# Kernel optimization log

Hardware: AMD Instinct MI355X
Metric: run time of the kernel (lower is better)

The kernel has to match this reference:

```python
import jax, jax.numpy as jnp
import numpy as np

NUM_HEADS = 8  # from init_kwargs

def _conv1x1(x, W, b):
    # x: [B, Cin, H, W], W: [Cout, Cin], b: [Cout]  (nn.Conv2d kernel_size=1)
    return jnp.einsum('bchw,oc->bohw', x, W) + b[None, :, None, None]

def setup_inputs() -> dict:
    key = jax.random.key(0)
    ks = jax.random.split(key, 9)
    B, C, H, W = 8, 256, 32, 32
    Ck, Cv, Co = 256, 256, 256
    s = 1.0 / np.sqrt(C)
    return {
        'x':  jax.random.normal(ks[0], (B, C, H, W), dtype=jnp.float32),
        'Wq': jax.random.normal(ks[1], (Ck, C), dtype=jnp.float32) * s,
        'bq': jax.random.normal(ks[2], (Ck,), dtype=jnp.float32) * 0.02,
        'Wk': jax.random.normal(ks[3], (Ck, C), dtype=jnp.float32) * s,
        'bk': jax.random.normal(ks[4], (Ck,), dtype=jnp.float32) * 0.02,
        'Wv': jax.random.normal(ks[5], (Cv, C), dtype=jnp.float32) * s,
        'bv': jax.random.normal(ks[6], (Cv,), dtype=jnp.float32) * 0.02,
        'Wo': jax.random.normal(ks[7], (Co, Cv), dtype=jnp.float32) * s,
        'bo': jax.random.normal(ks[8], (Co,), dtype=jnp.float32) * 0.02,
    }

def reference(x, Wq, bq, Wk, bk, Wv, bv, Wo, bo):
    B, C, H, W = x.shape
    q = _conv1x1(x, Wq, bq)  # [B, Ck, H, W]
    k = _conv1x1(x, Wk, bk)  # [B, Ck, H, W]
    v = _conv1x1(x, Wv, bv)  # [B, Cv, H, W]
    nh = NUM_HEADS
    dk = q.shape[1] // nh
    dv = v.shape[1] // nh
    N = H * W
    # split heads, flatten spatial dims into sequence
    q = q.reshape(B, nh, dk, N) * (dk ** -0.5)
    k = k.reshape(B, nh, dk, N)
    v = v.reshape(B, nh, dv, N)
    logits = jnp.einsum('bhdn,bhdm->bhnm', q, k)        # [B, nh, N, N]
    attn = jax.nn.softmax(logits, axis=-1)
    o = jnp.einsum('bhnm,bhdm->bhdn', attn, v)           # [B, nh, dv, N]
    o = o.reshape(B, nh * dv, H, W)
    return _conv1x1(o, Wo, bo)                           # [B, Co, H, W]
```

## Files before the change

### kernel.cpp

```cpp
#include <hip/hip_runtime.h>
#include <math.h>

typedef unsigned short u16;
typedef __attribute__((ext_vector_type(8))) unsigned short u16x8;
typedef __attribute__((ext_vector_type(8))) short s16x8;
typedef __attribute__((ext_vector_type(4))) float f32x4;

#define QK_SCALE (0.17677669529663687f * 1.4426950408889634f)

__device__ __forceinline__ unsigned cvt2(float lo, float hi) {
  unsigned r;
  asm("v_cvt_pk_bf16_f32 %0, %1, %2" : "=v"(r) : "v"(lo), "v"(hi));
  return r;
}
__device__ __forceinline__ u16 f2bf(float f) { return (u16)cvt2(f, f); }
__device__ __forceinline__ u16x8 ld16(const void* p) { u16x8 v; __builtin_memcpy(&v, p, 16); return v; }
__device__ __forceinline__ void st16(void* p, u16x8 v) { __builtin_memcpy(p, &v, 16); }
__device__ __forceinline__ void st4(void* p, unsigned v) { __builtin_memcpy(p, &v, 4); }
__device__ __forceinline__ void st8(void* p, unsigned lo, unsigned hi) {
  unsigned long long v = ((unsigned long long)hi << 32) | (unsigned long long)lo;
  __builtin_memcpy(p, &v, 8);
}
__device__ __forceinline__ f32x4 ldf4(const void* p) { f32x4 v; __builtin_memcpy(&v, p, 16); return v; }
__device__ __forceinline__ s16x8 frag16(const void* p) { s16x8 v; __builtin_memcpy(&v, p, 16); return v; }
__device__ __forceinline__ s16x8 pack8(f32x4 lo, f32x4 hi) {
  union { unsigned u[4]; s16x8 s; } c;
  c.u[0] = cvt2(lo.x, lo.y); c.u[1] = cvt2(lo.z, lo.w);
  c.u[2] = cvt2(hi.x, hi.y); c.u[3] = cvt2(hi.z, hi.w);
  return c.s;
}

__global__ __launch_bounds__(256) void r27_qkv(
    const float* __restrict__ x,
    const float* __restrict__ Wq, const float* __restrict__ bq,
    const float* __restrict__ Wk, const float* __restrict__ bk,
    const float* __restrict__ Wv, const float* __restrict__ bv,
    u16* __restrict__ qo, u16* __restrict__ ko, u16* __restrict__ vo)
{
  __shared__ u16 xt[64][264];
  __shared__ u16 wlds[192][40];

  const int t = threadIdx.x;
  const int ntile = blockIdx.x, hp = blockIdx.y, b = blockIdx.z;
  const int n0 = ntile * 64, h0 = hp * 2;
  const int w = t >> 6, lane = t & 63, l15 = lane & 15, quad = lane >> 4;
  const int oct = t & 7;

  {
    const int i = t & 15, co = t >> 4;
    const float* xb = x + ((size_t)b * 256 + co) * 1024 + n0 + i * 4;
    const int msk = (i & 7) << 3;
#pragma unroll
    for (int p = 0; p < 16; ++p) {
      const f32x4 a = ldf4(xb + (size_t)p * 16 * 1024);
      const int c = p * 16 + co;
#pragma unroll
      for (int j = 0; j < 4; ++j)
        xt[i * 4 + j][(c ^ msk)] = f2bf(a[j]);
    }
  }

  f32x4 acc[12];
#pragma unroll
  for (int i = 0; i < 12; ++i) acc[i] = (f32x4){0.f, 0.f, 0.f, 0.f};

  for (int ks = 0; ks < 8; ++ks) {
    __syncthreads();
    {
#pragma unroll
      for (int u = 0; u < 6; ++u) {
        const int row = (u * 256 + t) >> 3;
        const int m = row >> 6, hh = (row >> 5) & 1, rr = row & 31;
        const float* M = (m == 0) ? Wq : (m == 1) ? Wk : Wv;
        const f32x4 a = ldf4(M + (size_t)((h0 + hh) * 32 + rr) * 256
                             + ks * 32 + oct * 4);
        st8(&wlds[row][oct * 4], cvt2(a.x, a.y), cvt2(a.z, a.w));
      }
    }
    __syncthreads();

    const int nrow = w * 16 + l15;
    const s16x8 bfrag = frag16(
        &xt[nrow][(ks * 32 + quad * 8) ^ (((nrow >> 2) & 7) << 3)]);
#pragma unroll
    for (int mt = 0; mt < 12; ++mt) {
      const s16x8 af = frag16(&wlds[mt * 16 + l15][quad * 8]);
      acc[mt] = __builtin_amdgcn_mfma_f32_16x16x32_bf16(af, bfrag, acc[mt], 0, 0, 0);
    }
  }

  const int n = n0 + w * 16 + l15;
  const int sig = n & 127;
  const int ntn = sig >> 4, q4 = (sig >> 2) & 3, rn = sig & 3;
  const int nperm = (n & ~127) | ((ntn >> 1) << 5) | (q4 << 3) | ((ntn & 1) << 2) | rn;
#pragma unroll
  for (int hh = 0; hh < 2; ++hh) {
    const int h = h0 + hh;
    const size_t bh = (size_t)(b * 8 + h);
    u16* qrow = qo + (bh * 1024 + n) * 32;
    u16* krow = ko + (bh * 1024 + n) * 32;
#pragma unroll
    for (int half = 0; half < 2; ++half) {
      const int d0 = half * 16 + quad * 4;
      const f32x4 aq = acc[0 + hh * 2 + half];
      const f32x4 ak = acc[4 + hh * 2 + half];
      const f32x4 av = acc[8 + hh * 2 + half];
      st4(qrow + d0,     cvt2((aq.x + bq[h * 32 + d0 + 0]) * QK_SCALE,
                              (aq.y + bq[h * 32 + d0 + 1]) * QK_SCALE));
      st4(qrow + d0 + 2, cvt2((aq.z + bq[h * 32 + d0 + 2]) * QK_SCALE,
                              (aq.w + bq[h * 32 + d0 + 3]) * QK_SCALE));
      st4(krow + d0,     cvt2(ak.x + bk[h * 32 + d0 + 0],
                              ak.y + bk[h * 32 + d0 + 1]));
      st4(krow + d0 + 2, cvt2(ak.z + bk[h * 32 + d0 + 2],
                              ak.w + bk[h * 32 + d0 + 3]));
#pragma unroll
      for (int rr = 0; rr < 4; ++rr) {
        const int d = d0 + rr;
        vo[(bh * 32 + d) * 1024 + nperm] = f2bf(av[rr] + bv[h * 32 + d]);
      }
    }
  }
}

__global__ __launch_bounds__(256) void r27_attn(
    const u16* __restrict__ qw, const u16* __restrict__ kw,
    const u16* __restrict__ vw, u16* __restrict__ ows)
{
  __shared__ u16 klds[128][40];
  __shared__ u16 vlds[32][136];

  const int t = threadIdx.x;
  const int qtile = blockIdx.x;
  const int bh = blockIdx.y;
  const int w = t >> 6, lane = t & 63, l15 = lane & 15, quad = lane >> 4;

  const s16x8 qfrag = frag16(
      qw + ((size_t)bh * 1024 + qtile * 64 + w * 16 + l15) * 32 + quad * 8);

  const u16* kbase = kw + ((size_t)bh * 1024 + (t >> 1)) * 32 + (t & 1) * 16;
  const u16* vbase = vw + ((size_t)bh * 32 + (t >> 3)) * 1024 + (t & 7) * 16;

  u16x8 gk0 = ld16(kbase), gk1 = ld16(kbase + 8);
  u16x8 gv0 = ld16(vbase), gv1 = ld16(vbase + 8);

  f32x4 o0 = {0.f, 0.f, 0.f, 0.f}, o1 = {0.f, 0.f, 0.f, 0.f};
  float mrun = -1e30f, lrun = 0.f;

  for (int kb = 0; kb < 8; ++kb) {
    if (kb) __syncthreads();
    st16(&klds[t >> 1][(t & 1) * 16], gk0);
    st16(&klds[t >> 1][(t & 1) * 16 + 8], gk1);
    st16(&vlds[t >> 3][(t & 7) * 16], gv0);
    st16(&vlds[t >> 3][(t & 7) * 16 + 8], gv1);
    if (kb < 7) {
      const u16* kn = kbase + (size_t)(kb + 1) * (128 * 32);
      const u16* vn = vbase + (size_t)(kb + 1) * 128;
      gk0 = ld16(kn); gk1 = ld16(kn + 8);
      gv0 = ld16(vn); gv1 = ld16(vn + 8);
    }
    __syncthreads();

    f32x4 s[8];
    const f32x4 zz = {0.f, 0.f, 0.f, 0.f};
#pragma unroll
    for (int nt2 = 0; nt2 < 8; ++nt2) {
      const s16x8 kf = frag16(&klds[nt2 * 16 + l15][quad * 8]);
      s[nt2] = __builtin_amdgcn_mfma_f32_16x16x32_bf16(kf, qfrag, zz, 0, 0, 0);
    }

    float mx = fmaxf(fmaxf(s[0][0], s[0][1]), fmaxf(s[0][2], s[0][3]));
#pragma unroll
    for (int nt2 = 1; nt2 < 8; ++nt2)
      mx = fmaxf(mx, fmaxf(fmaxf(s[nt2][0], s[nt2][1]),
                           fmaxf(s[nt2][2], s[nt2][3])));
    mx = fmaxf(mx, __shfl_xor(mx, 16));
    mx = fmaxf(mx, __shfl_xor(mx, 32));
    const float mnew = fmaxf(mrun, mx);
    const float alpha = exp2f(mrun - mnew);
    float rs = 0.f;
#pragma unroll
    for (int nt2 = 0; nt2 < 8; ++nt2) {
#pragma unroll
      for (int r = 0; r < 4; ++r) {
        s[nt2][r] = exp2f(s[nt2][r] - mnew);
        rs += s[nt2][r];
      }
    }
    rs += __shfl_xor(rs, 16);
    rs += __shfl_xor(rs, 32);
    lrun = lrun * alpha + rs;
    mrun = mnew;
#pragma unroll
    for (int r = 0; r < 4; ++r) { o0[r] *= alpha; o1[r] *= alpha; }

#pragma unroll
    for (int ks = 0; ks < 4; ++ks) {
      const s16x8 pf  = pack8(s[2 * ks], s[2 * ks + 1]);
      const s16x8 vf0 = frag16(&vlds[l15][ks * 32 + quad * 8]);
      const s16x8 vf1 = frag16(&vlds[16 + l15][ks * 32 + quad * 8]);
      o0 = __builtin_amdgcn_mfma_f32_16x16x32_bf16(vf0, pf, o0, 0, 0, 0);
      o1 = __builtin_amdgcn_mfma_f32_16x16x32_bf16(vf1, pf, o1, 0, 0, 0);
    }
  }

  const float inv = 1.0f / lrun;
  const int b = bh >> 3, hh = bh & 7;
  u16* obase = ows + ((size_t)b * 1024 + qtile * 64 + w * 16 + l15) * 256
             + hh * 32 + quad * 4;
  st8(obase,      cvt2(o0[0] * inv, o0[1] * inv), cvt2(o0[2] * inv, o0[3] * inv));
  st8(obase + 16, cvt2(o1[0] * inv, o1[1] * inv), cvt2(o1[2] * inv, o1[3] * inv));
}

__global__ __launch_bounds__(256) void r27_oproj(
    const u16* __restrict__ ows,
    const float* __restrict__ Wo, const float* __restrict__ bo,
    float* __restrict__ out)
{
  __shared__ u16 o2t[32][256];
  __shared__ u16 wl3[2][256][40];

  const int t = threadIdx.x;
  const int nt = blockIdx.x, b = blockIdx.y;
  const int w = t >> 6, lane = t & 63, l15 = lane & 15, quad = lane >> 4;
  const int oct = t & 7;

  {
    const int g = t & 31, nr = t >> 5;
#pragma unroll
    for (int p = 0; p < 4; ++p) {
      const int n = p * 8 + nr;
      const u16* src = ows + ((size_t)b * 1024 + nt * 32 + n) * 256 + g * 8;
      st16(&o2t[n][(g ^ (n & 7)) << 3], ld16(src));
    }
  }

  auto stage_wo = [&](int ks, int buf) {
#pragma unroll
    for (int u = 0; u < 8; ++u) {
      const int row = u * 32 + (t >> 3);
      const f32x4 a = ldf4(Wo + (size_t)row * 256 + ks * 32 + oct * 4);
      st8(&wl3[buf][row][oct * 4], cvt2(a.x, a.y), cvt2(a.z, a.w));
    }
  };

  stage_wo(0, 0);
  __syncthreads();

  f32x4 acc[4][2];
#pragma unroll
  for (int mt = 0; mt < 4; ++mt) {
    acc[mt][0] = (f32x4){0.f, 0.f, 0.f, 0.f};
    acc[mt][1] = (f32x4){0.f, 0.f, 0.f, 0.f};
  }

  const int m0 = l15 & 7;

  for (int ks = 0; ks < 8; ++ks) {
    if (ks < 7) stage_wo(ks + 1, (ks + 1) & 1);
    const s16x8 b0 = frag16(&o2t[l15][((ks * 4 + quad) ^ m0) << 3]);
    const s16x8 b1 = frag16(&o2t[16 + l15][((ks * 4 + quad) ^ m0) << 3]);
#pragma unroll
    for (int mt = 0; mt < 4; ++mt) {
      const s16x8 af = frag16(&wl3[ks & 1][w * 64 + mt * 16 + l15][quad * 8]);
      acc[mt][0] = __builtin_amdgcn_mfma_f32_16x16x32_bf16(af, b0, acc[mt][0], 0, 0, 0);
      acc[mt][1] = __builtin_amdgcn_mfma_f32_16x16x32_bf16(af, b1, acc[mt][1], 0, 0, 0);
    }
    __syncthreads();
  }

#pragma unroll
  for (int mt = 0; mt < 4; ++mt) {
#pragma unroll
    for (int r = 0; r < 4; ++r) {
      const int oc = w * 64 + mt * 16 + quad * 4 + r;
      const float bov = bo[oc];
      out[((size_t)b * 256 + oc) * 1024 + nt * 32 + l15]      = acc[mt][0][r] + bov;
      out[((size_t)b * 256 + oc) * 1024 + nt * 32 + 16 + l15] = acc[mt][1][r] + bov;
    }
  }
}

extern "C" void kernel_launch(void* const* d_in, const int* in_sizes, int n_in,
                              void* d_out, int out_size, void* d_ws, size_t ws_size,
                              hipStream_t stream) {
  (void)in_sizes; (void)n_in; (void)out_size; (void)ws_size;
  const float* x  = (const float*)d_in[0];
  const float* Wq = (const float*)d_in[1];
  const float* bq = (const float*)d_in[2];
  const float* Wk = (const float*)d_in[3];
  const float* bk = (const float*)d_in[4];
  const float* Wv = (const float*)d_in[5];
  const float* bv = (const float*)d_in[6];
  const float* Wo = (const float*)d_in[7];
  const float* bo = (const float*)d_in[8];
  float* out = (float*)d_out;

  char* ws = (char*)d_ws;
  u16* qw  = (u16*)(ws);
  u16* kw  = (u16*)(ws + (4u << 20));
  u16* vw  = (u16*)(ws + (8u << 20));
  u16* ows = (u16*)(ws + (12u << 20));

  r27_qkv<<<dim3(16, 4, 8), 256, 0, stream>>>(
      x, Wq, bq, Wk, bk, Wv, bv, qw, kw, vw);
  r27_attn<<<dim3(16, 64), 256, 0, stream>>>(qw, kw, vw, ows);
  r27_oproj<<<dim3(32, 8), 256, 0, stream>>>(ows, Wo, bo, out);
}
```

Measured before the change: 128.1 us.

## Fuse output projection into attention kernel via last-arriver counter

Removes the separate output-projection launch. Each attention block bumps an atomic counter per (batch, query tile), and the eighth head block to arrive performs the Wo projection for that 64-column tile, reusing the shared memory. Wo staging moves from a double-buffered LDS scheme to register prefetch with a single LDS buffer. In exchange it adds a memset launch, threadfences and atomics, and leaves the projection work serialized on only 128 winning blocks at the tail of the attention kernel.

```diff
diff --git a/kernel.cpp b/kernel.cpp
--- a/kernel.cpp
+++ b/kernel.cpp
@@ -30,7 +30,7 @@
   return c.s;
 }
 
-__global__ __launch_bounds__(256) void r27_qkv(
+__global__ __launch_bounds__(256) void r28_qkv(
     const float* __restrict__ x,
     const float* __restrict__ Wq, const float* __restrict__ bq,
     const float* __restrict__ Wk, const float* __restrict__ bk,
@@ -122,12 +122,17 @@
   }
 }
 
-__global__ __launch_bounds__(256) void r27_attn(
+__global__ __launch_bounds__(256) void r28_attn_oproj(
     const u16* __restrict__ qw, const u16* __restrict__ kw,
-    const u16* __restrict__ vw, u16* __restrict__ ows)
+    const u16* __restrict__ vw,
+    const float* __restrict__ Wo, const float* __restrict__ bo,
+    u16* __restrict__ ows, float* __restrict__ out,
+    unsigned* __restrict__ cnt)
 {
-  __shared__ u16 klds[128][40];
-  __shared__ u16 vlds[32][136];
+  __shared__ __align__(16) char smem[36864];
+  __shared__ int winflag;
+  u16 (*klds)[40]  = (u16(*)[40])smem;
+  u16 (*vlds)[136] = (u16(*)[136])(smem + 10240);
 
   const int t = threadIdx.x;
   const int qtile = blockIdx.x;
@@ -209,73 +214,89 @@
              + hh * 32 + quad * 4;
   st8(obase,      cvt2(o0[0] * inv, o0[1] * inv), cvt2(o0[2] * inv, o0[3] * inv));
   st8(obase + 16, cvt2(o1[0] * inv, o1[1] * inv), cvt2(o1[2] * inv, o1[3] * inv));
-}
-
-__global__ __launch_bounds__(256) void r27_oproj(
-    const u16* __restrict__ ows,
-    const float* __restrict__ Wo, const float* __restrict__ bo,
-    float* __restrict__ out)
-{
-  __shared__ u16 o2t[32][256];
-  __shared__ u16 wl3[2][256][40];
-
-  const int t = threadIdx.x;
-  const int nt = blockIdx.x, b = blockIdx.y;
-  const int w = t >> 6, lane = t & 63, l15 = lane & 15, quad = lane >> 4;
-  const int oct = t & 7;
-
-  {
-    const int g = t & 31, nr = t >> 5;
-#pragma unroll
-    for (int p = 0; p < 4; ++p) {
-      const int n = p * 8 + nr;
-      const u16* src = ows + ((size_t)b * 1024 + nt * 32 + n) * 256 + g * 8;
-      st16(&o2t[n][(g ^ (n & 7)) << 3], ld16(src));
-    }
-  }
-
-  auto stage_wo = [&](int ks, int buf) {
+
+  __syncthreads();
+  __threadfence();
+  if (t == 0)
+    winflag = (atomicAdd(&cnt[b * 16 + qtile], 1u) == 7u) ? 1 : 0;
+  __syncthreads();
+  if (!winflag) return;
+  __threadfence();
+
+  u16 (*o2t)[256] = (u16(*)[256])smem;
+  u16 (*wl)[40]   = (u16(*)[40])(smem + 16384);
+
+  const int rr = t >> 3, oct = t & 7;
+  const float* wsrc = Wo + (size_t)rr * 256 + oct * 4;
+  const int m0 = l15 & 7;
+
+  for (int half = 0; half < 2; ++half) {
+    const int nt = qtile * 2 + half;
+    __syncthreads();
+    {
+      const int g = t & 31, nr = t >> 5;
+#pragma unroll
+      for (int p = 0; p < 4; ++p) {
+        const int n = p * 8 + nr;
+        const u16* src = ows + ((size_t)b * 1024 + nt * 32 + n) * 256 + g * 8;
+        st16(&o2t[n][(g ^ (n & 7)) << 3], ld16(src));
+      }
+    }
+    unsigned wreg[8][2];
 #pragma unroll
     for (int u = 0; u < 8; ++u) {
-      const int row = u * 32 + (t >> 3);
-      const f32x4 a = ldf4(Wo + (size_t)row * 256 + ks * 32 + oct * 4);
-      st8(&wl3[buf][row][oct * 4], cvt2(a.x, a.y), cvt2(a.z, a.w));
-    }
-  };
-
-  stage_wo(0, 0);
-  __syncthreads();
-
-  f32x4 acc[4][2];
-#pragma unroll
-  for (int mt = 0; mt < 4; ++mt) {
-    acc[mt][0] = (f32x4){0.f, 0.f, 0.f, 0.f};
-    acc[mt][1] = (f32x4){0.f, 0.f, 0.f, 0.f};
-  }
-
-  const int m0 = l15 & 7;
-
-  for (int ks = 0; ks < 8; ++ks) {
-    if (ks < 7) stage_wo(ks + 1, (ks + 1) & 1);
-    const s16x8 b0 = frag16(&o2t[l15][((ks * 4 + quad) ^ m0) << 3]);
-    const s16x8 b1 = frag16(&o2t[16 + l15][((ks * 4 + quad) ^ m0) << 3]);
+      const f32x4 a = ldf4(wsrc + (size_t)u * 32 * 256);
+      wreg[u][0] = cvt2(a.x, a.y); wreg[u][1] = cvt2(a.z, a.w);
+    }
+
+    f32x4 acc[4][2];
 #pragma unroll
     for (int mt = 0; mt < 4; ++mt) {
-      const s16x8 af = frag16(&wl3[ks & 1][w * 64 + mt * 16 + l15][quad * 8]);
-      acc[mt][0] = __builtin_amdgcn_mfma_f32_16x16x32_bf16(af, b0, acc[mt][0], 0, 0, 0);
-      acc[mt][1] = __builtin_amdgcn_mfma_f32_16x16x32_bf16(af, b1, acc[mt][1], 0, 0, 0);
-    }
-    __syncthreads();
-  }
-
-#pragma unroll
-  for (int mt = 0; mt < 4; ++mt) {
-#pragma unroll
-    for (int r = 0; r < 4; ++r) {
-      const int oc = w * 64 + mt * 16 + quad * 4 + r;
-      const float bov = bo[oc];
-      out[((size_t)b * 256 + oc) * 1024 + nt * 32 + l15]      = acc[mt][0][r] + bov;
-      out[((size_t)b * 256 + oc) * 1024 + nt * 32 + 16 + l15] = acc[mt][1][r] + bov;
+      acc[mt][0] = (f32x4){0.f, 0.f, 0.f, 0.f};
+      acc[mt][1] = (f32x4){0.f, 0.f, 0.f, 0.f};
+    }
+
+    for (int ks = 0; ks < 8; ++ks) {
+      __syncthreads();
+#pragma unroll
+      for (int u = 0; u < 8; ++u)
+        st8(&wl[u * 32 + rr][oct * 4], wreg[u][0], wreg[u][1]);
+      __syncthreads();
+
+      f32x4 nx[8];
+      if (ks < 7) {
+#pragma unroll
+        for (int u = 0; u < 8; ++u)
+          nx[u] = ldf4(wsrc + (size_t)u * 32 * 256 + (ks + 1) * 32);
+      }
+
+      const s16x8 b0 = frag16(&o2t[l15][((ks * 4 + quad) ^ m0) << 3]);
+      const s16x8 b1 = frag16(&o2t[16 + l15][((ks * 4 + quad) ^ m0) << 3]);
+#pragma unroll
+      for (int mt = 0; mt < 4; ++mt) {
+        const s16x8 af = frag16(&wl[w * 64 + mt * 16 + l15][quad * 8]);
+        acc[mt][0] = __builtin_amdgcn_mfma_f32_16x16x32_bf16(af, b0, acc[mt][0], 0, 0, 0);
+        acc[mt][1] = __builtin_amdgcn_mfma_f32_16x16x32_bf16(af, b1, acc[mt][1], 0, 0, 0);
+      }
+
+      if (ks < 7) {
+#pragma unroll
+        for (int u = 0; u < 8; ++u) {
+          wreg[u][0] = cvt2(nx[u].x, nx[u].y);
+          wreg[u][1] = cvt2(nx[u].z, nx[u].w);
+        }
+      }
+    }
+
+#pragma unroll
+    for (int mt = 0; mt < 4; ++mt) {
+#pragma unroll
+      for (int r = 0; r < 4; ++r) {
+        const int oc = w * 64 + mt * 16 + quad * 4 + r;
+        const float bov = bo[oc];
+        out[((size_t)b * 256 + oc) * 1024 + nt * 32 + l15]      = acc[mt][0][r] + bov;
+        out[((size_t)b * 256 + oc) * 1024 + nt * 32 + 16 + l15] = acc[mt][1][r] + bov;
+      }
     }
   }
 }
@@ -300,9 +321,11 @@
   u16* kw  = (u16*)(ws + (4u << 20));
   u16* vw  = (u16*)(ws + (8u << 20));
   u16* ows = (u16*)(ws + (12u << 20));
-
-  r27_qkv<<<dim3(16, 4, 8), 256, 0, stream>>>(
+  unsigned* cnt = (unsigned*)(ws + (16u << 20));
+
+  hipMemsetAsync(cnt, 0, 128 * sizeof(unsigned), stream);
+  r28_qkv<<<dim3(16, 4, 8), 256, 0, stream>>>(
       x, Wq, bq, Wk, bk, Wv, bv, qw, kw, vw);
-  r27_attn<<<dim3(16, 64), 256, 0, stream>>>(qw, kw, vw, ows);
-  r27_oproj<<<dim3(32, 8), 256, 0, stream>>>(ows, Wo, bo, out);
-}
+  r28_attn_oproj<<<dim3(16, 64), 256, 0, stream>>>(
+      qw, kw, vw, Wo, bo, ows, out, cnt);
+}
```

Measured after the change: 258.2 us. 2.02x slower.

## Split output projection across output-channel quarters and register-prefetch Wo tiles

Applied to the files above, without the earlier changes.

The oproj kernel grid gains a third dimension of 4, so each block computes 64 output channels instead of 256. This raises the block count from 256 to 1024 to fill more CUs. The shared Wo staging shrinks from a double-buffered 256-row tile to a single 64-row tile, and the next k-slice is prefetched into registers while the MFMAs run. The trade-off is that each block now reloads and transposes the same 32x256 activation tile into LDS, so activation traffic is 4x redundant, and each k-step adds a second barrier.

```diff
diff --git a/kernel.cpp b/kernel.cpp
--- a/kernel.cpp
+++ b/kernel.cpp
@@ -30,7 +30,7 @@
   return c.s;
 }
 
-__global__ __launch_bounds__(256) void r27_qkv(
+__global__ __launch_bounds__(256) void r29_qkv(
     const float* __restrict__ x,
     const float* __restrict__ Wq, const float* __restrict__ bq,
     const float* __restrict__ Wk, const float* __restrict__ bk,
@@ -122,7 +122,7 @@
   }
 }
 
-__global__ __launch_bounds__(256) void r27_attn(
+__global__ __launch_bounds__(256) void r29_attn(
     const u16* __restrict__ qw, const u16* __restrict__ kw,
     const u16* __restrict__ vw, u16* __restrict__ ows)
 {
@@ -211,18 +211,17 @@
   st8(obase + 16, cvt2(o1[0] * inv, o1[1] * inv), cvt2(o1[2] * inv, o1[3] * inv));
 }
 
-__global__ __launch_bounds__(256) void r27_oproj(
+__global__ __launch_bounds__(256) void r29_oproj(
     const u16* __restrict__ ows,
     const float* __restrict__ Wo, const float* __restrict__ bo,
     float* __restrict__ out)
 {
   __shared__ u16 o2t[32][256];
-  __shared__ u16 wl3[2][256][40];
+  __shared__ u16 wl[64][40];
 
   const int t = threadIdx.x;
-  const int nt = blockIdx.x, b = blockIdx.y;
+  const int nt = blockIdx.x, b = blockIdx.y, q = blockIdx.z;
   const int w = t >> 6, lane = t & 63, l15 = lane & 15, quad = lane >> 4;
-  const int oct = t & 7;
 
   {
     const int g = t & 31, nr = t >> 5;
@@ -234,49 +233,45 @@
     }
   }
 
-  auto stage_wo = [&](int ks, int buf) {
-#pragma unroll
-    for (int u = 0; u < 8; ++u) {
-      const int row = u * 32 + (t >> 3);
-      const f32x4 a = ldf4(Wo + (size_t)row * 256 + ks * 32 + oct * 4);
-      st8(&wl3[buf][row][oct * 4], cvt2(a.x, a.y), cvt2(a.z, a.w));
-    }
-  };
-
-  stage_wo(0, 0);
-  __syncthreads();
-
-  f32x4 acc[4][2];
-#pragma unroll
-  for (int mt = 0; mt < 4; ++mt) {
-    acc[mt][0] = (f32x4){0.f, 0.f, 0.f, 0.f};
-    acc[mt][1] = (f32x4){0.f, 0.f, 0.f, 0.f};
-  }
-
+  const int rl = t >> 2, cq = t & 3;
+  const float* wsrc = Wo + (size_t)(q * 64 + rl) * 256 + cq * 8;
+  unsigned wr0, wr1, wr2, wr3;
+  {
+    const f32x4 a = ldf4(wsrc), c = ldf4(wsrc + 4);
+    wr0 = cvt2(a.x, a.y); wr1 = cvt2(a.z, a.w);
+    wr2 = cvt2(c.x, c.y); wr3 = cvt2(c.z, c.w);
+  }
+
+  f32x4 acc0 = {0.f, 0.f, 0.f, 0.f}, acc1 = {0.f, 0.f, 0.f, 0.f};
   const int m0 = l15 & 7;
 
   for (int ks = 0; ks < 8; ++ks) {
-    if (ks < 7) stage_wo(ks + 1, (ks + 1) & 1);
+    __syncthreads();
+    st8(&wl[rl][cq * 8], wr0, wr1);
+    st8(&wl[rl][cq * 8 + 4], wr2, wr3);
+    __syncthreads();
+
+    f32x4 na, nc;
+    if (ks < 7) { na = ldf4(wsrc + (ks + 1) * 32); nc = ldf4(wsrc + (ks + 1) * 32 + 4); }
+
+    const s16x8 af = frag16(&wl[w * 16 + l15][quad * 8]);
     const s16x8 b0 = frag16(&o2t[l15][((ks * 4 + quad) ^ m0) << 3]);
     const s16x8 b1 = frag16(&o2t[16 + l15][((ks * 4 + quad) ^ m0) << 3]);
-#pragma unroll
-    for (int mt = 0; mt < 4; ++mt) {
-      const s16x8 af = frag16(&wl3[ks & 1][w * 64 + mt * 16 + l15][quad * 8]);
-      acc[mt][0] = __builtin_amdgcn_mfma_f32_16x16x32_bf16(af, b0, acc[mt][0], 0, 0, 0);
-      acc[mt][1] = __builtin_amdgcn_mfma_f32_16x16x32_bf16(af, b1, acc[mt][1], 0, 0, 0);
-    }
-    __syncthreads();
-  }
-
-#pragma unroll
-  for (int mt = 0; mt < 4; ++mt) {
-#pragma unroll
-    for (int r = 0; r < 4; ++r) {
-      const int oc = w * 64 + mt * 16 + quad * 4 + r;
-      const float bov = bo[oc];
-      out[((size_t)b * 256 + oc) * 1024 + nt * 32 + l15]      = acc[mt][0][r] + bov;
-      out[((size_t)b * 256 + oc) * 1024 + nt * 32 + 16 + l15] = acc[mt][1][r] + bov;
-    }
+    acc0 = __builtin_amdgcn_mfma_f32_16x16x32_bf16(af, b0, acc0, 0, 0, 0);
+    acc1 = __builtin_amdgcn_mfma_f32_16x16x32_bf16(af, b1, acc1, 0, 0, 0);
+
+    if (ks < 7) {
+      wr0 = cvt2(na.x, na.y); wr1 = cvt2(na.z, na.w);
+      wr2 = cvt2(nc.x, nc.y); wr3 = cvt2(nc.z, nc.w);
+    }
+  }
+
+#pragma unroll
+  for (int r = 0; r < 4; ++r) {
+    const int oc = q * 64 + w * 16 + quad * 4 + r;
+    const float bov = bo[oc];
+    out[((size_t)b * 256 + oc) * 1024 + nt * 32 + l15]      = acc0[r] + bov;
+    out[((size_t)b * 256 + oc) * 1024 + nt * 32 + 16 + l15] = acc1[r] + bov;
   }
 }
 
@@ -301,8 +296,8 @@
   u16* vw  = (u16*)(ws + (8u << 20));
   u16* ows = (u16*)(ws + (12u << 20));
 
-  r27_qkv<<<dim3(16, 4, 8), 256, 0, stream>>>(
+  r29_qkv<<<dim3(16, 4, 8), 256, 0, stream>>>(
       x, Wq, bq, Wk, bk, Wv, bv, qw, kw, vw);
-  r27_attn<<<dim3(16, 64), 256, 0, stream>>>(qw, kw, vw, ows);
-  r27_oproj<<<dim3(32, 8), 256, 0, stream>>>(ows, Wo, bo, out);
-}
+  r29_attn<<<dim3(16, 64), 256, 0, stream>>>(qw, kw, vw, ows);
+  r29_oproj<<<dim3(32, 8, 4), 256, 0, stream>>>(ows, Wo, bo, out);
+}
```

Result: no change. 127.4 us (-0.6%).
